# Kernel optimization log

Measured on AMD Instinct MI355X. Metric: run time of the kernel, lower is better.

## Reference

```python
import jax, jax.numpy as jnp
import numpy as np

B, L, DIM = 2, 2048, 1024
H, D = 16, 64  # n_heads, head_dim; H*D == DIM


def setup_inputs() -> dict:
    key = jax.random.key(0)
    ks = jax.random.split(key, 5)
    s = 0.02
    return {
        "x": jax.random.normal(ks[0], (B, L, DIM), dtype=jnp.float32),
        "Wq": jax.random.normal(ks[1], (DIM, H * D), dtype=jnp.float32) * s,
        "Wk": jax.random.normal(ks[2], (DIM, H * D), dtype=jnp.float32) * s,
        "Wv": jax.random.normal(ks[3], (DIM, H * D), dtype=jnp.float32) * s,
        "Wo": jax.random.normal(ks[4], (H * D, DIM), dtype=jnp.float32) * s,
    }


def reference(x, Wq, Wk, Wv, Wo):
    b, l, _ = x.shape
    scale = 1.0 / np.sqrt(D).astype(np.float32)
    # QKV projections -> [b, h, l, d]
    q = (x @ Wq).reshape(b, l, H, D).transpose(0, 2, 1, 3)
    k = (x @ Wk).reshape(b, l, H, D).transpose(0, 2, 1, 3)
    v = (x @ Wv).reshape(b, l, H, D).transpose(0, 2, 1, 3)
    # dense scores [b, h, l, l]
    scores = jnp.einsum("bhqd,bhkd->bhqk", q, k)
    # diagonal mask: each token cannot attend to itself
    diag = jnp.eye(l, dtype=bool)  # [l, l]
    scores = jnp.where(diag, -jnp.inf, scores)
    attn = jax.nn.softmax(scores * scale, axis=-1)
    out = jnp.einsum("bhqk,bhkd->bhqd", attn, v)
    out = out.transpose(0, 2, 1, 3).reshape(b, l, H * D)
    return out @ Wo
```

## Files before the change

kernel.cpp:

```cpp
#include <hip/hip_runtime.h>
#include <hip/hip_bf16.h>
#include <math.h>

#define L_SEQ 2048
#define DIMN  1024
#define NH    16
#define HD    64
#define NB    2
#define NTOK  (NB * L_SEQ)

typedef __attribute__((ext_vector_type(8))) short bf16x8;
typedef __attribute__((ext_vector_type(4))) float f32x4;
typedef __attribute__((ext_vector_type(16))) float f32x16;
typedef __attribute__((ext_vector_type(4))) short short4v;
typedef __attribute__((ext_vector_type(2))) unsigned uint32x2;

__device__ __forceinline__ short f2bf(float x) {
  return (short)__bfloat16_as_ushort(__float2bfloat16(x));
}
__device__ __forceinline__ float bf2f(short x) {
  union { unsigned u; float f; } c;
  c.u = ((unsigned)(unsigned short)x) << 16;
  return c.f;
}

__device__ __forceinline__ unsigned cvt_pk_bf16(float lo, float hi) {
  unsigned r;
  asm("v_cvt_pk_bf16_f32 %0, %1, %2" : "=v"(r) : "v"(lo), "v"(hi));
  return r;
}

__device__ __forceinline__ void permlane32_swap(unsigned& a, unsigned& b) {
  asm volatile("v_permlane32_swap_b32 %0, %1" : "+v"(a), "+v"(b));
}

__device__ __forceinline__ void gload_lds16(const short* gsrc, char* lds_dst) {
  __builtin_amdgcn_global_load_lds(
      (const __attribute__((address_space(1))) void*)gsrc,
      (__attribute__((address_space(3))) void*)lds_dst, 16, 0, 0);
}

__global__ __launch_bounds__(256) void prep_k(const float* __restrict__ x,
                                              const float* __restrict__ Wq,
                                              const float* __restrict__ Wk,
                                              const float* __restrict__ Wv,
                                              const float* __restrict__ Wo,
                                              short* __restrict__ xb,
                                              short* __restrict__ Wqt,
                                              short* __restrict__ Wkt,
                                              short* __restrict__ Wvt,
                                              short* __restrict__ Wot) {
  const int tid = threadIdx.x;
  if (blockIdx.z == 0) {
    const int id = blockIdx.x + 16 * blockIdx.y;
#pragma unroll
    for (int rep = 0; rep < 8; ++rep) {
      const size_t i = ((size_t)(id + rep * 256)) * 2048 + tid * 8;
      float4 a = *(const float4*)(x + i);
      float4 b = *(const float4*)(x + i + 4);
      bf16x8 o;
      o[0] = f2bf(a.x); o[1] = f2bf(a.y); o[2] = f2bf(a.z); o[3] = f2bf(a.w);
      o[4] = f2bf(b.x); o[5] = f2bf(b.y); o[6] = f2bf(b.z); o[7] = f2bf(b.w);
      *(bf16x8*)(xb + i) = o;
    }
    return;
  }
  const float* W  = (blockIdx.z == 1) ? Wq : (blockIdx.z == 2) ? Wk
                    : (blockIdx.z == 3) ? Wv : Wo;
  short* Wt = (blockIdx.z == 1) ? Wqt : (blockIdx.z == 2) ? Wkt
              : (blockIdx.z == 3) ? Wvt : Wot;
  __shared__ float s[64][65];
  const int k0 = blockIdx.y * 64, n0 = blockIdx.x * 64;
#pragma unroll
  for (int i = 0; i < 4; ++i) {
    int idx = i * 256 + tid;
    int r = idx >> 4, c = (idx & 15) * 4;
    float4 v = *(const float4*)(W + (size_t)(k0 + r) * DIMN + n0 + c);
    s[r][c] = v.x; s[r][c + 1] = v.y; s[r][c + 2] = v.z; s[r][c + 3] = v.w;
  }
  __syncthreads();
#pragma unroll
  for (int i = 0; i < 4; ++i) {
    int idx = i * 256 + tid;
    int r = idx >> 4, c = (idx & 15) * 4;
    short4v o = { f2bf(s[c][r]), f2bf(s[c + 1][r]), f2bf(s[c + 2][r]), f2bf(s[c + 3][r]) };
    *(short4v*)(Wt + (size_t)(n0 + r) * DIMN + k0 + c) = o;
  }
}

__global__ __launch_bounds__(256) void vT_k(const short* __restrict__ V,
                                            short* __restrict__ Vt) {
  __shared__ short s[64][72];
  const int tid = threadIdx.x;
  const int bh = blockIdx.y;
  const int l0 = blockIdx.x * 64;
  const int row = tid >> 2, c0 = (tid & 3) * 16;
  const short* Vh = V + (size_t)bh * L_SEQ * HD;
  bf16x8 a = *(const bf16x8*)(Vh + (size_t)(l0 + row) * HD + c0);
  bf16x8 b = *(const bf16x8*)(Vh + (size_t)(l0 + row) * HD + c0 + 8);
#pragma unroll
  for (int j = 0; j < 8; ++j) { s[c0 + j][row] = a[j]; s[c0 + 8 + j][row] = b[j]; }
  __syncthreads();
  short* Vth = Vt + (size_t)bh * HD * L_SEQ;
  bf16x8 o0 = *(const bf16x8*)&s[row][c0];
  bf16x8 o1 = *(const bf16x8*)&s[row][c0 + 8];
  *(bf16x8*)(Vth + (size_t)row * L_SEQ + l0 + c0) = o0;
  *(bf16x8*)(Vth + (size_t)row * L_SEQ + l0 + c0 + 8) = o1;
}

template <int MODE>
__global__ __launch_bounds__(256) void mm_k(const short* __restrict__ A,
                                            const short* __restrict__ B0,
                                            const short* __restrict__ B1,
                                            const short* __restrict__ B2,
                                            void* __restrict__ C0,
                                            void* __restrict__ C1,
                                            void* __restrict__ C2,
                                            float scale0) {
  __shared__ char smem[65536];
  const int tid  = threadIdx.x;
  const int lane = tid & 63, wv = tid >> 6;
  const int g = lane >> 4, r16 = lane & 15;
  const int wr = wv >> 1, wc = wv & 1;
  const int row0 = blockIdx.y * 128, col0 = blockIdx.x * 128;
  const int z = blockIdx.z;
  const short* Bt = (z == 0) ? B0 : (z == 1 ? B1 : B2);
  const float scale = (MODE == 0 && z == 0) ? scale0 : 1.0f;

  f32x4 acc[4][4];
#pragma unroll
  for (int mi = 0; mi < 4; ++mi)
#pragma unroll
    for (int ni = 0; ni < 4; ++ni) acc[mi][ni] = (f32x4){0.f, 0.f, 0.f, 0.f};

  auto stage = [&](int buf, int kt) {
    const int k0 = kt * 64;
    char* As = smem + buf * 32768;
    char* Bs = As + 16384;
#pragma unroll
    for (int j = 0; j < 4; ++j) {
      const int o = j * 4096 + wv * 1024 + lane * 16;
      const int row = o >> 7;
      const int slot = (o >> 4) & 7;
      const int ksrc = k0 + ((slot ^ (row & 7)) << 3);
      gload_lds16(A  + (size_t)(row0 + row) * DIMN + ksrc, As + j * 4096 + wv * 1024);
      gload_lds16(Bt + (size_t)(col0 + row) * DIMN + ksrc, Bs + j * 4096 + wv * 1024);
    }
  };

  auto compute = [&](int buf) {
    const char* As = smem + buf * 32768;
    const char* Bs = As + 16384;
#pragma unroll
    for (int ks = 0; ks < 2; ++ks) {
      bf16x8 a[4], b[4];
#pragma unroll
      for (int mi = 0; mi < 4; ++mi) {
        const int row = wr * 64 + mi * 16 + r16;
        const int slot = (ks * 4 + g) ^ (row & 7);
        a[mi] = *(const bf16x8*)(As + row * 128 + slot * 16);
      }
#pragma unroll
      for (int ni = 0; ni < 4; ++ni) {
        const int row = wc * 64 + ni * 16 + r16;
        const int slot = (ks * 4 + g) ^ (row & 7);
        b[ni] = *(const bf16x8*)(Bs + row * 128 + slot * 16);
      }
#pragma unroll
      for (int mi = 0; mi < 4; ++mi)
#pragma unroll
        for (int ni = 0; ni < 4; ++ni)
          acc[mi][ni] = __builtin_amdgcn_mfma_f32_16x16x32_bf16(a[mi], b[ni], acc[mi][ni], 0, 0, 0);
    }
  };

  stage(0, 0);
  __syncthreads();
  int cur = 0;
  for (int kt = 0; kt < DIMN / 64 - 1; ++kt) {
    stage(cur ^ 1, kt + 1);
    compute(cur);
    __syncthreads();
    cur ^= 1;
  }
  compute(cur);

  void* Cp = (z == 0) ? C0 : (z == 1 ? C1 : C2);
#pragma unroll
  for (int mi = 0; mi < 4; ++mi) {
#pragma unroll
    for (int reg = 0; reg < 4; ++reg) {
      const int t = row0 + wr * 64 + mi * 16 + 4 * g + reg;
#pragma unroll
      for (int ni = 0; ni < 4; ++ni) {
        const int n = col0 + wc * 64 + ni * 16 + r16;
        if (MODE == 0) {
          const int b = t >> 11, l = t & (L_SEQ - 1);
          const int h = n >> 6, d = n & 63;
          ((short*)Cp)[(((size_t)(b * NH + h)) * L_SEQ + l) * HD + d] =
              f2bf(acc[mi][ni][reg] * scale);
        } else {
          ((float*)Cp)[(size_t)t * DIMN + n] = acc[mi][ni][reg];
        }
      }
    }
  }
}

__global__ __launch_bounds__(256) void mm64_k(const short* __restrict__ A,
                                              const short* __restrict__ Bt,
                                              float* __restrict__ C) {
  __shared__ char smem[49152];
  const int tid  = threadIdx.x;
  const int lane = tid & 63, wv = tid >> 6;
  const int g = lane >> 4, r16 = lane & 15;
  const int row0 = blockIdx.y * 64, col0 = blockIdx.x * 128;

  f32x4 acc[4][2];
#pragma unroll
  for (int mi = 0; mi < 4; ++mi)
#pragma unroll
    for (int ni = 0; ni < 2; ++ni) acc[mi][ni] = (f32x4){0.f, 0.f, 0.f, 0.f};

  auto stage = [&](int buf, int kt) {
    const int k0 = kt * 64;
    char* As = smem + buf * 24576;
    char* Bs = As + 8192;
#pragma unroll
    for (int j = 0; j < 2; ++j) {
      const int o = j * 4096 + wv * 1024 + lane * 16;
      const int row = o >> 7;
      const int slot = (o >> 4) & 7;
      const int ksrc = k0 + ((slot ^ (row & 7)) << 3);
      gload_lds16(A + (size_t)(row0 + row) * DIMN + ksrc, As + j * 4096 + wv * 1024);
    }
#pragma unroll
    for (int j = 0; j < 4; ++j) {
      const int o = j * 4096 + wv * 1024 + lane * 16;
      const int row = o >> 7;
      const int slot = (o >> 4) & 7;
      const int ksrc = k0 + ((slot ^ (row & 7)) << 3);
      gload_lds16(Bt + (size_t)(col0 + row) * DIMN + ksrc, Bs + j * 4096 + wv * 1024);
    }
  };

  auto compute = [&](int buf) {
    const char* As = smem + buf * 24576;
    const char* Bs = As + 8192;
#pragma unroll
    for (int ks = 0; ks < 2; ++ks) {
      bf16x8 a[4], b[2];
#pragma unroll
      for (int mi = 0; mi < 4; ++mi) {
        const int row = mi * 16 + r16;
        const int slot = (ks * 4 + g) ^ (row & 7);
        a[mi] = *(const bf16x8*)(As + row * 128 + slot * 16);
      }
#pragma unroll
      for (int ni = 0; ni < 2; ++ni) {
        const int row = wv * 32 + ni * 16 + r16;
        const int slot = (ks * 4 + g) ^ (row & 7);
        b[ni] = *(const bf16x8*)(Bs + row * 128 + slot * 16);
      }
#pragma unroll
      for (int mi = 0; mi < 4; ++mi)
#pragma unroll
        for (int ni = 0; ni < 2; ++ni)
          acc[mi][ni] = __builtin_amdgcn_mfma_f32_16x16x32_bf16(a[mi], b[ni], acc[mi][ni], 0, 0, 0);
    }
  };

  stage(0, 0);
  __syncthreads();
  int cur = 0;
  for (int kt = 0; kt < DIMN / 64 - 1; ++kt) {
    stage(cur ^ 1, kt + 1);
    compute(cur);
    __syncthreads();
    cur ^= 1;
  }
  compute(cur);

#pragma unroll
  for (int mi = 0; mi < 4; ++mi) {
#pragma unroll
    for (int reg = 0; reg < 4; ++reg) {
      const int t = row0 + mi * 16 + 4 * g + reg;
#pragma unroll
      for (int ni = 0; ni < 2; ++ni) {
        const int n = col0 + wv * 32 + ni * 16 + r16;
        C[(size_t)t * DIMN + n] = acc[mi][ni][reg];
      }
    }
  }
}

__global__ __launch_bounds__(256) void attn_k(const short* __restrict__ Q,
                                              const short* __restrict__ K,
                                              const short* __restrict__ Vt,
                                              short* __restrict__ Op0,
                                              short* __restrict__ Op1,
                                              float* __restrict__ Lp) {
  __shared__ char kv[2][16384];

  const int tid  = threadIdx.x;
  const int wave = tid >> 6, lane = tid & 63;
  const int h = lane >> 5, r32 = lane & 31;

  const int id = blockIdx.x + 32 * blockIdx.y;
  const int j8 = id >> 3;
  const int bh = (id & 7) * 4 + (j8 >> 5);
  const int qtile = (j8 >> 1) & 15;
  const int split = j8 & 1;

  const int qbase = qtile * 128 + wave * 32;
  const int dtile = qtile * 2 + (wave >> 1);
  const int qg = qbase + r32;
  const int kbase = split * 16;

  const short* Qh  = Q  + (size_t)bh * L_SEQ * HD;
  const short* Kh  = K  + (size_t)bh * L_SEQ * HD;
  const short* Vth = Vt + (size_t)bh * HD * L_SEQ;

  bf16x8 qv[4];
#pragma unroll
  for (int ks = 0; ks < 4; ++ks)
    qv[ks] = *(const bf16x8*)(Qh + (size_t)qg * HD + ks * 16 + 8 * h);

  float lsum = 0.f;
  f32x16 o32[2];
#pragma unroll
  for (int db = 0; db < 2; ++db)
#pragma unroll
    for (int r = 0; r < 16; ++r) o32[db][r] = 0.f;

  const int sw = r32 & 7;
  const int rbase = r32 * 128;

  const int si1 = 256 + tid;
  const int row0s = tid >> 3,  c0s = (((tid & 7) ^ (row0s & 7)) << 3);
  const int row1s = si1 >> 3,  c1s = (((si1 & 7) ^ (row1s & 7)) << 3);
  const short* kp0 = Kh + (size_t)(split * 1024 + row0s) * HD + c0s;
  const short* kp1 = Kh + (size_t)(split * 1024 + row1s) * HD + c1s;
  const short* vp0 = Vth + (size_t)row0s * L_SEQ + split * 1024 + c0s;
  const short* vp1 = Vth + (size_t)row1s * L_SEQ + split * 1024 + c1s;
  const int ldo0 = tid * 16, ldo1 = si1 * 16;

  auto stage = [&](char* base) {
    gload_lds16(kp0, base + ldo0);
    gload_lds16(kp1, base + ldo1);
    gload_lds16(vp0, base + 8192 + ldo0);
    gload_lds16(vp1, base + 8192 + ldo1);
    kp0 += 64 * HD;
    kp1 += 64 * HD;
    vp0 += 64;
    vp1 += 64;
  };

  auto compute = [&](const char* Kb, int kt) {
    const char* Vb = Kb + 8192;

    f32x16 sa[2];
#pragma unroll
    for (int kb = 0; kb < 2; ++kb)
#pragma unroll
      for (int r = 0; r < 16; ++r) sa[kb][r] = 0.f;
    __builtin_amdgcn_s_setprio(1);
#pragma unroll
    for (int kb = 0; kb < 2; ++kb)
#pragma unroll
      for (int ks = 0; ks < 4; ++ks) {
        bf16x8 ak = *(const bf16x8*)(Kb + (kb * 32) * 128 + rbase + ((2 * ks + h) ^ sw) * 16);
        sa[kb] = __builtin_amdgcn_mfma_f32_32x32x16_bf16(ak, qv[ks], sa[kb], 0, 0, 0);
      }
    __builtin_amdgcn_s_setprio(0);

    if (kt == dtile) {
      const int tgt = qg - kt * 64;
#pragma unroll
      for (int kb = 0; kb < 2; ++kb)
#pragma unroll
        for (int r = 0; r < 16; ++r)
          if (kb * 32 + (r & 3) + 8 * (r >> 2) + 4 * h == tgt) sa[kb][r] = -INFINITY;
    }

#pragma unroll
    for (int kb = 0; kb < 2; ++kb)
#pragma unroll
      for (int r = 0; r < 16; ++r) sa[kb][r] = __builtin_amdgcn_exp2f(sa[kb][r]);
    float ps = 0.f;
#pragma unroll
    for (int kb = 0; kb < 2; ++kb) {
      float u0 = (sa[kb][0] + sa[kb][1]) + (sa[kb][2] + sa[kb][3]);
      float u1 = (sa[kb][4] + sa[kb][5]) + (sa[kb][6] + sa[kb][7]);
      float u2 = (sa[kb][8] + sa[kb][9]) + (sa[kb][10] + sa[kb][11]);
      float u3 = (sa[kb][12] + sa[kb][13]) + (sa[kb][14] + sa[kb][15]);
      ps += (u0 + u1) + (u2 + u3);
    }
    lsum += ps;

    bf16x8 bp[4];
#pragma unroll
    for (int kk = 0; kk < 4; ++kk) {
      const int kb = kk >> 1, s8 = (kk & 1) * 8;
      unsigned lo0 = cvt_pk_bf16(sa[kb][s8 + 0], sa[kb][s8 + 1]);
      unsigned lo1 = cvt_pk_bf16(sa[kb][s8 + 2], sa[kb][s8 + 3]);
      unsigned hi0 = cvt_pk_bf16(sa[kb][s8 + 4], sa[kb][s8 + 5]);
      unsigned hi1 = cvt_pk_bf16(sa[kb][s8 + 6], sa[kb][s8 + 7]);
      permlane32_swap(lo0, hi0);
      permlane32_swap(lo1, hi1);
      union { unsigned w[4]; bf16x8 v; } u;
      u.w[0] = lo0; u.w[1] = lo1; u.w[2] = hi0; u.w[3] = hi1;
      bp[kk] = u.v;
    }

    __builtin_amdgcn_s_setprio(1);
#pragma unroll
    for (int kk = 0; kk < 4; ++kk)
#pragma unroll
      for (int db = 0; db < 2; ++db) {
        bf16x8 av = *(const bf16x8*)(Vb + (db * 32) * 128 + rbase + ((2 * kk + h) ^ sw) * 16);
        o32[db] = __builtin_amdgcn_mfma_f32_32x32x16_bf16(av, bp[kk], o32[db], 0, 0, 0);
      }
    __builtin_amdgcn_s_setprio(0);
  };

#define STEP(CBUF, SBUF, KT, DO_STAGE)                        \
  do {                                                        \
    asm volatile("s_waitcnt vmcnt(0)" ::: "memory");          \
    __builtin_amdgcn_s_barrier();                             \
    __builtin_amdgcn_sched_barrier(0);                        \
    if (DO_STAGE) stage(SBUF);                                \
    compute(CBUF, KT);                                        \
  } while (0)

  stage(kv[0]);
  for (int i = 0; i < 14; i += 2) {
    STEP(kv[0], kv[1], kbase + i,     true);
    STEP(kv[1], kv[0], kbase + i + 1, true);
  }
  STEP(kv[0], kv[1], kbase + 14, true);
  STEP(kv[1], kv[0], kbase + 15, false);
#undef STEP

  lsum += __shfl_xor(lsum, 32);

  short* Opart = split ? Op1 : Op0;
  const size_t rowO = ((size_t)bh * L_SEQ + qg) * HD;
#pragma unroll
  for (int db = 0; db < 2; ++db)
#pragma unroll
    for (int grp = 0; grp < 4; ++grp) {
      const int d0 = db * 32 + grp * 8 + 4 * h;
      uint32x2 ow = { cvt_pk_bf16(o32[db][grp * 4 + 0], o32[db][grp * 4 + 1]),
                      cvt_pk_bf16(o32[db][grp * 4 + 2], o32[db][grp * 4 + 3]) };
      *(uint32x2*)(Opart + rowO + d0) = ow;
    }
  if (h == 0)
    Lp[(size_t)(split * NB * NH + bh) * L_SEQ + qg] = lsum;
}

__global__ __launch_bounds__(256) void combine_k(const short* __restrict__ Op0,
                                                 const short* __restrict__ Op1,
                                                 const float* __restrict__ Lp,
                                                 short* __restrict__ AO) {
  const int idx = blockIdx.x * 256 + threadIdx.x;
  const int d8 = (idx & 7) * 8;
  const int q  = (idx >> 3) & (L_SEQ - 1);
  const int bh = idx >> 14;
  const size_t po = ((size_t)bh * L_SEQ + q) * HD + d8;
  bf16x8 p0 = *(const bf16x8*)(Op0 + po);
  bf16x8 p1 = *(const bf16x8*)(Op1 + po);
  const float l0 = Lp[(size_t)bh * L_SEQ + q];
  const float l1 = Lp[(size_t)(NB * NH + bh) * L_SEQ + q];
  const float inv = 1.0f / (l0 + l1);
  const int b = bh >> 4, hh = bh & 15;
  bf16x8 o;
#pragma unroll
  for (int j = 0; j < 8; ++j)
    o[j] = f2bf((bf2f(p0[j]) + bf2f(p1[j])) * inv);
  *(bf16x8*)(AO + ((size_t)(b * L_SEQ + q)) * DIMN + hh * HD + d8) = o;
}

extern "C" void kernel_launch(void* const* d_in, const int* in_sizes, int n_in,
                              void* d_out, int out_size, void* d_ws, size_t ws_size,
                              hipStream_t stream) {
  const float* x  = (const float*)d_in[0];
  const float* Wq = (const float*)d_in[1];
  const float* Wk = (const float*)d_in[2];
  const float* Wv = (const float*)d_in[3];
  const float* Wo = (const float*)d_in[4];
  float* out = (float*)d_out;

  short* xb  = (short*)d_ws;
  short* Wqt = xb  + (size_t)NTOK * DIMN;
  short* Wkt = Wqt + (size_t)DIMN * DIMN;
  short* Wvt = Wkt + (size_t)DIMN * DIMN;
  short* Wot = Wvt + (size_t)DIMN * DIMN;
  short* Qb  = Wot + (size_t)DIMN * DIMN;
  short* Kb  = Qb  + (size_t)NTOK * DIMN;
  short* Vb  = Kb  + (size_t)NTOK * DIMN;
  short* Vtb = Vb  + (size_t)NTOK * DIMN;
  short* AO  = Vtb + (size_t)NTOK * DIMN;
  float* Lp  = (float*)(AO + (size_t)NTOK * DIMN);
  short* Op0 = xb;
  short* Op1 = Vb;

  prep_k<<<dim3(16, 16, 5), 256, 0, stream>>>(x, Wq, Wk, Wv, Wo,
                                              xb, Wqt, Wkt, Wvt, Wot);

  mm_k<0><<<dim3(DIMN / 128, NTOK / 128, 3), 256, 0, stream>>>(
      xb, Wqt, Wkt, Wvt, Qb, Kb, Vb, 0.125f * 1.4426950408889634f);

  vT_k<<<dim3(L_SEQ / 64, NB * NH), 256, 0, stream>>>(Vb, Vtb);

  attn_k<<<dim3(32, NB * NH), 256, 0, stream>>>(Qb, Kb, Vtb, Op0, Op1, Lp);

  combine_k<<<2048, 256, 0, stream>>>(Op0, Op1, Lp, AO);

  mm64_k<<<dim3(DIMN / 128, NTOK / 64), 256, 0, stream>>>(AO, Wot, out);
}
```

Measured before the change: 120.3 us.

## Single-buffer QKV GEMM LDS and drop setprio hints in attention

```diff
diff --git a/kernel.cpp b/kernel.cpp
--- a/kernel.cpp
+++ b/kernel.cpp
@@ -108,16 +108,15 @@
   *(bf16x8*)(Vth + (size_t)row * L_SEQ + l0 + c0 + 8) = o1;
 }
 
-template <int MODE>
 __global__ __launch_bounds__(256) void mm_k(const short* __restrict__ A,
                                             const short* __restrict__ B0,
                                             const short* __restrict__ B1,
                                             const short* __restrict__ B2,
-                                            void* __restrict__ C0,
-                                            void* __restrict__ C1,
-                                            void* __restrict__ C2,
+                                            short* __restrict__ C0,
+                                            short* __restrict__ C1,
+                                            short* __restrict__ C2,
                                             float scale0) {
-  __shared__ char smem[65536];
+  __shared__ char smem[32768];
   const int tid  = threadIdx.x;
   const int lane = tid & 63, wv = tid >> 6;
   const int g = lane >> 4, r16 = lane & 15;
@@ -125,7 +124,7 @@
   const int row0 = blockIdx.y * 128, col0 = blockIdx.x * 128;
   const int z = blockIdx.z;
   const short* Bt = (z == 0) ? B0 : (z == 1 ? B1 : B2);
-  const float scale = (MODE == 0 && z == 0) ? scale0 : 1.0f;
+  const float scale = (z == 0) ? scale0 : 1.0f;
 
   f32x4 acc[4][4];
 #pragma unroll
@@ -133,10 +132,10 @@
 #pragma unroll
     for (int ni = 0; ni < 4; ++ni) acc[mi][ni] = (f32x4){0.f, 0.f, 0.f, 0.f};
 
-  auto stage = [&](int buf, int kt) {
+  auto stage = [&](int kt) {
     const int k0 = kt * 64;
-    char* As = smem + buf * 32768;
-    char* Bs = As + 16384;
+    char* As = smem;
+    char* Bs = smem + 16384;
 #pragma unroll
     for (int j = 0; j < 4; ++j) {
       const int o = j * 4096 + wv * 1024 + lane * 16;
@@ -148,9 +147,9 @@
     }
   };
 
-  auto compute = [&](int buf) {
-    const char* As = smem + buf * 32768;
-    const char* Bs = As + 16384;
+  auto compute = [&]() {
+    const char* As = smem;
+    const char* Bs = smem + 16384;
 #pragma unroll
     for (int ks = 0; ks < 2; ++ks) {
       bf16x8 a[4], b[4];
@@ -174,18 +173,16 @@
     }
   };
 
-  stage(0, 0);
-  __syncthreads();
-  int cur = 0;
-  for (int kt = 0; kt < DIMN / 64 - 1; ++kt) {
-    stage(cur ^ 1, kt + 1);
-    compute(cur);
+  for (int kt = 0; kt < DIMN / 64; ++kt) {
+    stage(kt);
+    asm volatile("s_waitcnt vmcnt(0)" ::: "memory");
+    __builtin_amdgcn_s_barrier();
+    __builtin_amdgcn_sched_barrier(0);
+    compute();
     __syncthreads();
-    cur ^= 1;
-  }
-  compute(cur);
-
-  void* Cp = (z == 0) ? C0 : (z == 1 ? C1 : C2);
+  }
+
+  short* Cp = (z == 0) ? C0 : (z == 1 ? C1 : C2);
 #pragma unroll
   for (int mi = 0; mi < 4; ++mi) {
 #pragma unroll
@@ -194,14 +191,10 @@
 #pragma unroll
       for (int ni = 0; ni < 4; ++ni) {
         const int n = col0 + wc * 64 + ni * 16 + r16;
-        if (MODE == 0) {
-          const int b = t >> 11, l = t & (L_SEQ - 1);
-          const int h = n >> 6, d = n & 63;
-          ((short*)Cp)[(((size_t)(b * NH + h)) * L_SEQ + l) * HD + d] =
-              f2bf(acc[mi][ni][reg] * scale);
-        } else {
-          ((float*)Cp)[(size_t)t * DIMN + n] = acc[mi][ni][reg];
-        }
+        const int b = t >> 11, l = t & (L_SEQ - 1);
+        const int h = n >> 6, d = n & 63;
+        Cp[(((size_t)(b * NH + h)) * L_SEQ + l) * HD + d] =
+            f2bf(acc[mi][ni][reg] * scale);
       }
     }
   }
@@ -365,7 +358,6 @@
     for (int kb = 0; kb < 2; ++kb)
 #pragma unroll
       for (int r = 0; r < 16; ++r) sa[kb][r] = 0.f;
-    __builtin_amdgcn_s_setprio(1);
 #pragma unroll
     for (int kb = 0; kb < 2; ++kb)
 #pragma unroll
@@ -373,7 +365,6 @@
         bf16x8 ak = *(const bf16x8*)(Kb + (kb * 32) * 128 + rbase + ((2 * ks + h) ^ sw) * 16);
         sa[kb] = __builtin_amdgcn_mfma_f32_32x32x16_bf16(ak, qv[ks], sa[kb], 0, 0, 0);
       }
-    __builtin_amdgcn_s_setprio(0);
 
     if (kt == dtile) {
       const int tgt = qg - kt * 64;
@@ -414,7 +405,6 @@
       bp[kk] = u.v;
     }
 
-    __builtin_amdgcn_s_setprio(1);
 #pragma unroll
     for (int kk = 0; kk < 4; ++kk)
 #pragma unroll
@@ -422,7 +412,6 @@
         bf16x8 av = *(const bf16x8*)(Vb + (db * 32) * 128 + rbase + ((2 * kk + h) ^ sw) * 16);
         o32[db] = __builtin_amdgcn_mfma_f32_32x32x16_bf16(av, bp[kk], o32[db], 0, 0, 0);
       }
-    __builtin_amdgcn_s_setprio(0);
   };
 
 #define STEP(CBUF, SBUF, KT, DO_STAGE)                        \
@@ -509,7 +498,7 @@
   prep_k<<<dim3(16, 16, 5), 256, 0, stream>>>(x, Wq, Wk, Wv, Wo,
                                               xb, Wqt, Wkt, Wvt, Wot);
 
-  mm_k<0><<<dim3(DIMN / 128, NTOK / 128, 3), 256, 0, stream>>>(
+  mm_k<<<dim3(DIMN / 128, NTOK / 128, 3), 256, 0, stream>>>(
       xb, Wqt, Wkt, Wvt, Qb, Kb, Vb, 0.125f * 1.4426950408889634f);
 
   vT_k<<<dim3(L_SEQ / 64, NB * NH), 256, 0, stream>>>(Vb, Vtb);
```

Result: slower. 124.5 us (+3.5%).
